# Kernel optimization log

Hardware: AMD Instinct MI355X
Metric: run time of the kernel (lower is better)

Reference implementation:

```python
import jax, jax.numpy as jnp
import numpy as np

B, T, N, F, D, E = 8, 256, 118, 3, 128, 372
G = B * T  # number of graphs after flattening batch*time


def _gcn(x, src, dst, W, b):
    # x: [G, N, Fin] -> PyG GCNConv: X' = D^-1/2 (A+I) D^-1/2 (X W) + b
    h = x @ W  # [G, N, Fout]
    deg = jnp.ones((N,), h.dtype).at[dst].add(1.0)  # in-degree + self loop
    inv = deg ** -0.5
    norm = inv[src] * inv[dst]  # [E]
    agg = h * (1.0 / deg)[None, :, None]  # self-loop term: inv[i]*inv[i] = 1/deg
    agg = agg.at[:, dst].add(h[:, src] * norm[None, :, None])
    return agg + b


def _lstm_layer(x, Wih, Whh, bih, bhh):
    # x: [B, T, I]; PyTorch gate order i, f, g, o
    Bb, H = x.shape[0], Whh.shape[1]
    h0 = jnp.zeros((Bb, H), x.dtype)
    c0 = jnp.zeros((Bb, H), x.dtype)

    def step(carry, xt):
        h, c = carry
        gates = xt @ Wih.T + h @ Whh.T + bih + bhh
        i, f, g, o = jnp.split(gates, 4, axis=-1)
        c = jax.nn.sigmoid(f) * c + jax.nn.sigmoid(i) * jnp.tanh(g)
        h = jax.nn.sigmoid(o) * jnp.tanh(c)
        return (h, c), h

    _, ys = jax.lax.scan(step, (h0, c0), jnp.swapaxes(x, 0, 1))
    return jnp.swapaxes(ys, 0, 1)


def setup_inputs() -> dict:
    key = jax.random.key(0)
    ks = jax.random.split(key, 24)
    s = 0.05

    def rn(i, shape):
        return jax.random.normal(ks[i], shape, jnp.float32) * s

    return {
        "snapshot_sequence": jax.random.normal(ks[0], (B, T, N, F), jnp.float32),
        "edge_index": jax.random.randint(ks[1], (2, E), 0, N, dtype=jnp.int64),
        "scale": jnp.ones((F,), jnp.float32),
        "shift": jnp.zeros((F,), jnp.float32),
        "W1": rn(2, (F, D)), "b1": jnp.zeros((D,), jnp.float32),
        "W2": rn(3, (D, D)), "b2": jnp.zeros((D,), jnp.float32),
        "W3": rn(4, (D, D)), "b3": jnp.zeros((D,), jnp.float32),
        "Wih0": rn(5, (4 * D, D)), "Whh0": rn(6, (4 * D, D)),
        "bih0": jnp.zeros((4 * D,), jnp.float32), "bhh0": jnp.zeros((4 * D,), jnp.float32),
        "Wih1": rn(7, (4 * D, D)), "Whh1": rn(8, (4 * D, D)),
        "bih1": jnp.zeros((4 * D,), jnp.float32), "bhh1": jnp.zeros((4 * D,), jnp.float32),
        "hW1": rn(9, (D, 128)), "hb1": jnp.zeros((128,), jnp.float32),
        "hW2": rn(10, (128, 64)), "hb2": jnp.zeros((64,), jnp.float32),
        "hW3": rn(11, (64, 2)), "hb3": jnp.zeros((2,), jnp.float32),
    }


def reference(snapshot_sequence, edge_index, scale, shift,
              W1, b1, W2, b2, W3, b3,
              Wih0, Whh0, bih0, bhh0, Wih1, Whh1, bih1, bhh1,
              hW1, hb1, hW2, hb2, hW3, hb3):
    src, dst = edge_index[0], edge_index[1]
    x = snapshot_sequence * scale + shift              # FeatureNormalizer
    x = x.reshape(G, N, F)                             # flatten batch*time graphs
    x = jax.nn.silu(_gcn(x, src, dst, W1, b1))         # GCNConv 1 (dropout = eval identity)
    x = jax.nn.silu(_gcn(x, src, dst, W2, b2))         # GCNConv 2
    x = jax.nn.silu(_gcn(x, src, dst, W3, b3))         # GCNConv 3
    emb = x.mean(axis=1)                               # global_mean_pool -> [G, D]
    emb = emb.reshape(B, T, D)
    h = _lstm_layer(emb, Wih0, Whh0, bih0, bhh0)       # 2-layer LSTM (eval: no dropout)
    h = _lstm_layer(h, Wih1, Whh1, bih1, bhh1)
    final = h[:, -1, :]                                # [B, D]
    y = jax.nn.silu(final @ hW1 + hb1)
    y = jax.nn.silu(y @ hW2 + hb2)
    y = y @ hW3 + hb3
    return jax.nn.softplus(y) + 1e-6                   # [B, 2]
```

## Files before the change

### kernel.cpp

```cpp
#include <hip/hip_runtime.h>
#include <math.h>

#define NN 118
#define EE 372
#define GG 2048
#define DD 128
#define TT 256
#define BB 8
#define FD 512

#define XS 136

typedef short bf16x8 __attribute__((ext_vector_type(8)));
typedef float f32x4  __attribute__((ext_vector_type(4)));
typedef _Float16 f16x2 __attribute__((ext_vector_type(2)));

__device__ __forceinline__ float frcp_(float x) { return __builtin_amdgcn_rcpf(x); }
__device__ __forceinline__ float sig_f(float x) { return frcp_(1.0f + __expf(-x)); }
__device__ __forceinline__ float tanh_f(float x) { return 1.0f - 2.0f * frcp_(__expf(2.0f * x) + 1.0f); }
__device__ __forceinline__ float silu_f(float x) { return x * frcp_(1.0f + __expf(-x)); }
__device__ __forceinline__ float siluf_(float x) { return x / (1.0f + expf(-x)); }

__device__ __forceinline__ float fdot2_(unsigned int a, unsigned int b, float c) {
#if defined(__has_builtin) && __has_builtin(__builtin_amdgcn_fdot2)
    return __builtin_amdgcn_fdot2(__builtin_bit_cast(f16x2, a),
                                  __builtin_bit_cast(f16x2, b), c, false);
#else
    f16x2 x = __builtin_bit_cast(f16x2, a), y = __builtin_bit_cast(f16x2, b);
    return c + (float)x[0] * (float)y[0] + (float)x[1] * (float)y[1];
#endif
}

__device__ __forceinline__ void bar_lds() {
    asm volatile("s_waitcnt lgkmcnt(0)\n\ts_barrier" ::: "memory");
}

__device__ __forceinline__ unsigned short f2bf(float x) {
    unsigned int u = __float_as_uint(x);
    unsigned int r = (u + 0x7fffu + ((u >> 16) & 1u)) >> 16;
    return (unsigned short)r;
}
__device__ __forceinline__ float bf2f(unsigned short b) {
    return __uint_as_float(((unsigned int)b) << 16);
}

__global__ void prep_kernel(const int* __restrict__ ei,
                            const float* __restrict__ bih0, const float* __restrict__ bhh0,
                            const float* __restrict__ bih1, const float* __restrict__ bhh1,
                            float* __restrict__ bias0, float* __restrict__ bias1,
                            unsigned short* __restrict__ AbG) {
    __shared__ int sflag;
    __shared__ int ssrc[EE], sdst[EE];
    __shared__ int scount[NN];
    __shared__ float sinv[NN];
    __shared__ float Adense[NN * NN];
    int tid = threadIdx.x;
    if (tid == 0) sflag = 0;
    __syncthreads();
    for (int i = tid; i < 2 * EE; i += blockDim.x)
        if ((i & 1) && ei[i] != 0) atomicOr(&sflag, 1);
    __syncthreads();
    bool m64 = (sflag == 0);
    for (int e = tid; e < EE; e += blockDim.x) {
        int s, d;
        if (m64) { s = ei[2 * e]; d = ei[2 * EE + 2 * e]; }
        else     { s = ei[e];     d = ei[EE + e]; }
        s = min(max(s, 0), NN - 1); d = min(max(d, 0), NN - 1);
        ssrc[e] = s; sdst[e] = d;
    }
    for (int n = tid; n < NN; n += blockDim.x) scount[n] = 0;
    for (int i = tid; i < NN * NN; i += blockDim.x) Adense[i] = 0.0f;
    __syncthreads();
    for (int e = tid; e < EE; e += blockDim.x) atomicAdd(&scount[sdst[e]], 1);
    __syncthreads();
    for (int n = tid; n < NN; n += blockDim.x) {
        float deg = 1.0f + (float)scount[n];
        sinv[n] = rsqrtf(deg);
        Adense[n * NN + n] = 1.0f / deg;
    }
    __syncthreads();
    for (int e = tid; e < EE; e += blockDim.x)
        atomicAdd(&Adense[sdst[e] * NN + ssrc[e]], sinv[ssrc[e]] * sinv[sdst[e]]);
    __syncthreads();
    for (int i = tid; i < 128 * 128; i += blockDim.x) {
        int r = i >> 7, c = i & 127;
        AbG[i] = (r < NN && c < NN) ? f2bf(Adense[r * NN + c]) : (unsigned short)0;
    }
    for (int j = tid; j < FD; j += blockDim.x) {
        bias0[j] = bih0[j] + bhh0[j];
        bias1[j] = bih1[j] + bhh1[j];
    }
}

__global__ void convw_kernel(const float* __restrict__ W, unsigned short* __restrict__ out) {
    int i = blockIdx.x * 512 + threadIdx.x;
    int n = i >> 7, k = i & 127;
    out[i] = f2bf(W[k * DD + n]);
}

__global__ void convh_kernel(const float* __restrict__ W, unsigned int* __restrict__ out) {
    int i = blockIdx.x * 512 + threadIdx.x;
    int d = i & 127;
    int rest = i >> 7;
    int quarter = rest & 3;
    int qg = rest >> 2;
    int q = qg & 15, g = qg >> 4;
    const float* row = W + (size_t)(g * 128 + d) * 128 + quarter * 32;
    float a = row[2 * q], b = row[2 * q + 1];
    unsigned short lo = __builtin_bit_cast(unsigned short, (_Float16)a);
    unsigned short hi = __builtin_bit_cast(unsigned short, (_Float16)b);
    out[i] = (unsigned int)lo | ((unsigned int)hi << 16);
}

__global__ void transpose_kernel(const float* __restrict__ in, float* __restrict__ out) {
    int idx = blockIdx.x * blockDim.x + threadIdx.x;
    int j = idx >> 7, k = idx & 127;
    out[k * FD + j] = in[idx];
}

__device__ __forceinline__ void load_m(const unsigned short* __restrict__ src,
                                       unsigned short* __restrict__ dst, int tid) {
    const uint4* s4 = (const uint4*)src;
    for (int c = tid; c < 2048; c += 512) {
        int r = c >> 4, k8 = (c & 15) * 8;
        uint4 v = s4[c];
        *(uint4*)(dst + r * XS + k8) = v;
    }
}

__device__ __forceinline__ void mm_xw(const unsigned short* __restrict__ xb,
                                      const unsigned short* __restrict__ wt,
                                      unsigned short* __restrict__ hS, int tid) {
    int lane = tid & 63, w = tid >> 6;
    int lm = lane & 15, lq = lane >> 4;
    int wm = (w & 1) * 64, wn = (w >> 1) * 32;
    f32x4 acc[4][2];
#pragma unroll
    for (int mt = 0; mt < 4; ++mt)
#pragma unroll
        for (int nt = 0; nt < 2; ++nt) acc[mt][nt] = (f32x4){0.f, 0.f, 0.f, 0.f};
#pragma unroll
    for (int kb = 0; kb < 4; ++kb) {
        int ko = kb * 32 + lq * 8;
        bf16x8 b0 = *(const bf16x8*)(wt + (wn + lm) * XS + ko);
        bf16x8 b1 = *(const bf16x8*)(wt + (wn + 16 + lm) * XS + ko);
#pragma unroll
        for (int mt = 0; mt < 4; ++mt) {
            bf16x8 af = *(const bf16x8*)(xb + (wm + mt * 16 + lm) * XS + ko);
            acc[mt][0] = __builtin_amdgcn_mfma_f32_16x16x32_bf16(af, b0, acc[mt][0], 0, 0, 0);
            acc[mt][1] = __builtin_amdgcn_mfma_f32_16x16x32_bf16(af, b1, acc[mt][1], 0, 0, 0);
        }
    }
#pragma unroll
    for (int mt = 0; mt < 4; ++mt)
#pragma unroll
        for (int nt = 0; nt < 2; ++nt) {
            f32x4 a = acc[mt][nt];
            ushort4 pk;
            pk.x = f2bf(a[0]); pk.y = f2bf(a[1]); pk.z = f2bf(a[2]); pk.w = f2bf(a[3]);
            *(ushort4*)(hS + (wn + nt * 16 + lm) * XS + wm + mt * 16 + lq * 4) = pk;
        }
}

__device__ __forceinline__ void mm_agg(const unsigned short* __restrict__ Ab,
                                       const unsigned short* __restrict__ hS,
                                       unsigned short* __restrict__ xb,
                                       float bn0, float bn1, int tid) {
    int lane = tid & 63, w = tid >> 6;
    int lm = lane & 15, lq = lane >> 4;
    int wm = (w & 1) * 64, wn = (w >> 1) * 32;
    f32x4 acc[4][2];
#pragma unroll
    for (int mt = 0; mt < 4; ++mt)
#pragma unroll
        for (int nt = 0; nt < 2; ++nt) acc[mt][nt] = (f32x4){0.f, 0.f, 0.f, 0.f};
#pragma unroll
    for (int kb = 0; kb < 4; ++kb) {
        int ko = kb * 32 + lq * 8;
        bf16x8 b0 = *(const bf16x8*)(hS + (wn + lm) * XS + ko);
        bf16x8 b1 = *(const bf16x8*)(hS + (wn + 16 + lm) * XS + ko);
#pragma unroll
        for (int mt = 0; mt < 4; ++mt) {
            bf16x8 af = *(const bf16x8*)(Ab + (wm + mt * 16 + lm) * XS + ko);
            acc[mt][0] = __builtin_amdgcn_mfma_f32_16x16x32_bf16(af, b0, acc[mt][0], 0, 0, 0);
            acc[mt][1] = __builtin_amdgcn_mfma_f32_16x16x32_bf16(af, b1, acc[mt][1], 0, 0, 0);
        }
    }
#pragma unroll
    for (int mt = 0; mt < 4; ++mt)
#pragma unroll
        for (int nt = 0; nt < 2; ++nt) {
            float bn = nt ? bn1 : bn0;
            int col = wn + nt * 16 + lm;
#pragma unroll
            for (int i = 0; i < 4; ++i) {
                float v = silu_f(acc[mt][nt][i] + bn);
                xb[(wm + mt * 16 + lq * 4 + i) * XS + col] = f2bf(v);
            }
        }
}

__global__ __launch_bounds__(512) void gcn_kernel(
    const float* __restrict__ xg, const float* __restrict__ scale, const float* __restrict__ shift,
    const float* __restrict__ W1, const float* __restrict__ b1,
    const float* __restrict__ b2, const float* __restrict__ b3,
    const unsigned short* __restrict__ AbG,
    const unsigned short* __restrict__ Wt2g, const unsigned short* __restrict__ Wt3g,
    float* __restrict__ emb) {
    extern __shared__ char smem[];
    unsigned short* xb = (unsigned short*)smem;
    unsigned short* hS = (unsigned short*)(smem + 34816);
    unsigned short* Ab = (unsigned short*)(smem + 69632);
    unsigned short* wt = (unsigned short*)(smem + 104448);
    float* xinL  = (float*)(smem + 139264);
    float* meanS = (float*)(smem + 140688);
    int tid = threadIdx.x;
    int lane = tid & 63, w = tid >> 6;
    int g = blockIdx.x;

    for (int i = tid; i < 2176; i += 512) ((uint4*)hS)[i] = (uint4){0, 0, 0, 0};
    for (int i = tid; i < 170; i += 512) ((uint4*)(xb + NN * XS))[i] = (uint4){0, 0, 0, 0};
    float s0 = scale[0], s1 = scale[1], s2 = scale[2];
    float t0 = shift[0], t1 = shift[1], t2 = shift[2];
    const float* xrow = xg + (size_t)g * (NN * 3);
    for (int i = tid; i < NN * 3; i += 512) {
        int f = i % 3;
        float sc = (f == 0) ? s0 : ((f == 1) ? s1 : s2);
        float sf = (f == 0) ? t0 : ((f == 1) ? t1 : t2);
        xinL[i] = xrow[i] * sc + sf;
    }
    load_m(AbG, Ab, tid);
    load_m(Wt2g, wt, tid);
    int lm = lane & 15;
    int wn = (w >> 1) * 32;
    int n0 = wn + lm, n1 = wn + 16 + lm;
    float b1a = b1[n0], b1b = b1[n1];
    float b2a = b2[n0], b2b = b2[n1];
    float b3a = b3[n0], b3b = b3[n1];
    int dd = lane * 2;
    float2 w10 = *(const float2*)(W1 + dd);
    float2 w11 = *(const float2*)(W1 + DD + dd);
    float2 w12 = *(const float2*)(W1 + 2 * DD + dd);
    bar_lds();
    for (int k = 0; k < 15; ++k) {
        int n = w + 8 * k;
        if (n >= NN) break;
        float x0 = xinL[n * 3], x1 = xinL[n * 3 + 1], x2 = xinL[n * 3 + 2];
        hS[dd * XS + n]       = f2bf(x0 * w10.x + x1 * w11.x + x2 * w12.x);
        hS[(dd + 1) * XS + n] = f2bf(x0 * w10.y + x1 * w11.y + x2 * w12.y);
    }
    bar_lds();
    mm_agg(Ab, hS, xb, b1a, b1b, tid);
    bar_lds();
    mm_xw(xb, wt, hS, tid);
    bar_lds();
    load_m(Wt3g, wt, tid);
    mm_agg(Ab, hS, xb, b2a, b2b, tid);
    bar_lds();
    mm_xw(xb, wt, hS, tid);
    bar_lds();
    mm_agg(Ab, hS, xb, b3a, b3b, tid);
    bar_lds();
    {
        int d = tid & 127, part = tid >> 7;
        int a0 = part * 30;
        int a1 = (a0 + 30 < NN) ? (a0 + 30) : NN;
        float s = 0.f;
        for (int n = a0; n < a1; ++n) s += bf2f(xb[n * XS + d]);
        meanS[part * 128 + d] = s;
    }
    bar_lds();
    if (tid < 128) {
        float s = meanS[tid] + meanS[128 + tid] + meanS[256 + tid] + meanS[384 + tid];
        emb[(size_t)g * DD + tid] = s * (1.0f / (float)NN);
    }
}

__global__ __launch_bounds__(512) void proj_kernel(const float* __restrict__ src,
                                                   const float* __restrict__ WT,
                                                   const float* __restrict__ bias,
                                                   float* __restrict__ dst) {
    __shared__ __align__(16) float eL[DD];
    int g = blockIdx.x, tid = threadIdx.x;
    if (tid < DD) eL[tid] = src[(size_t)g * DD + tid];
    __syncthreads();
    float acc = bias[tid];
    const float* wt = WT + tid;
#pragma unroll 8
    for (int k = 0; k < DD; ++k) acc += eL[k] * wt[(size_t)k * FD];
    dst[(size_t)g * FD + tid] = acc;
}

__global__ __launch_bounds__(512, 2) void scan_kernel(
    const float* __restrict__ inp,
    const unsigned int* __restrict__ Wc,
    float* __restrict__ hout, int full) {
    __shared__ __align__(16) unsigned short hL[DD];
    __shared__ __align__(16) float sgP[3 * DD * 4];
    int b = blockIdx.x, j = threadIdx.x;
    int d = j & 127, quarter = j >> 7;
    unsigned int wreg[4][16];
#pragma unroll
    for (int g = 0; g < 4; ++g)
#pragma unroll
        for (int q = 0; q < 16; ++q)
            wreg[g][q] = Wc[(((g * 16 + q) << 2) + quarter) * 128 + d];
#pragma unroll
    for (int g = 0; g < 4; ++g)
#pragma unroll
        for (int q = 0; q < 16; ++q)
            asm volatile("" : "+v"(wreg[g][q]));
    if (j < 64) ((unsigned int*)hL)[j] = 0u;
    float creg = 0.f;
    const float* ib = inp + (size_t)b * TT * FD;
    float* hb_ = hout + (size_t)b * (full ? TT * DD : DD);
    float xg0[4], xg1[4];
    if (quarter == 0) {
#pragma unroll
        for (int g = 0; g < 4; ++g) { xg0[g] = ib[g * DD + d]; xg1[g] = ib[FD + g * DD + d]; }
    }
    bar_lds();
    for (int t = 0; t < TT; ++t) {
        float xg2[4];
        if (quarter == 0) {
            bool more = (t + 2 < TT);
#pragma unroll
            for (int g = 0; g < 4; ++g)
                xg2[g] = more ? ib[(t + 2) * FD + g * DD + d] : 0.f;
        }
        const uint4* h4 = (const uint4*)(hL + quarter * 32);
        float a0 = 0.f, a1 = 0.f, a2 = 0.f, a3 = 0.f;
#pragma unroll
        for (int c = 0; c < 4; ++c) {
            uint4 hv = h4[c];
            a0 = fdot2_(wreg[0][4 * c + 0], hv.x, a0);
            a1 = fdot2_(wreg[1][4 * c + 0], hv.x, a1);
            a2 = fdot2_(wreg[2][4 * c + 0], hv.x, a2);
            a3 = fdot2_(wreg[3][4 * c + 0], hv.x, a3);
            a0 = fdot2_(wreg[0][4 * c + 1], hv.y, a0);
            a1 = fdot2_(wreg[1][4 * c + 1], hv.y, a1);
            a2 = fdot2_(wreg[2][4 * c + 1], hv.y, a2);
            a3 = fdot2_(wreg[3][4 * c + 1], hv.y, a3);
            a0 = fdot2_(wreg[0][4 * c + 2], hv.z, a0);
            a1 = fdot2_(wreg[1][4 * c + 2], hv.z, a1);
            a2 = fdot2_(wreg[2][4 * c + 2], hv.z, a2);
            a3 = fdot2_(wreg[3][4 * c + 2], hv.z, a3);
            a0 = fdot2_(wreg[0][4 * c + 3], hv.w, a0);
            a1 = fdot2_(wreg[1][4 * c + 3], hv.w, a1);
            a2 = fdot2_(wreg[2][4 * c + 3], hv.w, a2);
            a3 = fdot2_(wreg[3][4 * c + 3], hv.w, a3);
        }
        if (quarter != 0)
            *(float4*)(sgP + ((quarter - 1) * DD + d) * 4) = make_float4(a0, a1, a2, a3);
        bar_lds();
        if (quarter == 0) {
            float4 p1 = *(const float4*)(sgP + d * 4);
            float4 p2 = *(const float4*)(sgP + (DD + d) * 4);
            float4 p3 = *(const float4*)(sgP + (2 * DD + d) * 4);
            float iv = sig_f(a0 + p1.x + p2.x + p3.x + xg0[0]);
            float fv = sig_f(a1 + p1.y + p2.y + p3.y + xg0[1]);
            float gv = tanh_f(a2 + p1.z + p2.z + p3.z + xg0[2]);
            float ov = sig_f(a3 + p1.w + p2.w + p3.w + xg0[3]);
            float cn = fv * creg + iv * gv;
            creg = cn;
            float hn = ov * tanh_f(cn);
            ((_Float16*)hL)[d] = (_Float16)hn;
            if (full) hb_[t * DD + d] = hn;
            else if (t == TT - 1) hb_[d] = hn;
#pragma unroll
            for (int g = 0; g < 4; ++g) { xg0[g] = xg1[g]; xg1[g] = xg2[g]; }
        }
        bar_lds();
    }
}

__global__ void head_kernel(const float* __restrict__ hfin,
                            const float* __restrict__ hW1, const float* __restrict__ hb1,
                            const float* __restrict__ hW2, const float* __restrict__ hb2,
                            const float* __restrict__ hW3, const float* __restrict__ hb3,
                            float* __restrict__ out) {
    __shared__ float fh[BB * DD];
    __shared__ float y1[BB * DD];
    __shared__ float y2[BB * 64];
    int tid = threadIdx.x;
    for (int i = tid; i < BB * DD; i += 256) fh[i] = hfin[i];
    __syncthreads();
    for (int i = tid; i < BB * DD; i += 256) {
        int bb = i >> 7, jj = i & 127;
        float acc = hb1[jj];
        for (int k = 0; k < DD; ++k) acc += fh[(bb << 7) + k] * hW1[(k << 7) + jj];
        y1[i] = siluf_(acc);
    }
    __syncthreads();
    for (int i = tid; i < BB * 64; i += 256) {
        int bb = i >> 6, jj = i & 63;
        float acc = hb2[jj];
        for (int k = 0; k < DD; ++k) acc += y1[(bb << 7) + k] * hW2[(k << 6) + jj];
        y2[i] = siluf_(acc);
    }
    __syncthreads();
    if (tid < BB * 2) {
        int bb = tid >> 1, m = tid & 1;
        float acc = hb3[m];
        for (int k = 0; k < 64; ++k) acc += y2[(bb << 6) + k] * hW3[k * 2 + m];
        float sp = fmaxf(acc, 0.f) + log1pf(expf(-fabsf(acc)));
        out[tid] = sp + 1e-6f;
    }
}

extern "C" void kernel_launch(void* const* d_in, const int* in_sizes, int n_in,
                              void* d_out, int out_size, void* d_ws, size_t ws_size,
                              hipStream_t stream) {
    const float* snap  = (const float*)d_in[0];
    const int*   edges = (const int*)d_in[1];
    const float* scale = (const float*)d_in[2];
    const float* shift = (const float*)d_in[3];
    const float* W1 = (const float*)d_in[4];
    const float* b1 = (const float*)d_in[5];
    const float* W2 = (const float*)d_in[6];
    const float* b2 = (const float*)d_in[7];
    const float* W3 = (const float*)d_in[8];
    const float* b3 = (const float*)d_in[9];
    const float* Wih0 = (const float*)d_in[10];
    const float* Whh0 = (const float*)d_in[11];
    const float* bih0 = (const float*)d_in[12];
    const float* bhh0 = (const float*)d_in[13];
    const float* Wih1 = (const float*)d_in[14];
    const float* Whh1 = (const float*)d_in[15];
    const float* bih1 = (const float*)d_in[16];
    const float* bhh1 = (const float*)d_in[17];
    const float* hW1 = (const float*)d_in[18];
    const float* hb1 = (const float*)d_in[19];
    const float* hW2 = (const float*)d_in[20];
    const float* hb2 = (const float*)d_in[21];
    const float* hW3 = (const float*)d_in[22];
    const float* hb3 = (const float*)d_in[23];

    float* ws = (float*)d_ws;
    float* bias0 = ws + 0;
    float* bias1 = ws + 512;
    unsigned short* AbG  = (unsigned short*)(ws + 1024);
    unsigned short* Wt2g = (unsigned short*)(ws + 9216);
    unsigned short* Wt3g = (unsigned short*)(ws + 17408);
    float* WT0 = ws + 25600;
    float* WT1 = ws + 91136;
    unsigned int* Wc0 = (unsigned int*)(ws + 156672);
    unsigned int* Wc1 = (unsigned int*)(ws + 189440);
    float* emb   = ws + 222208;
    float* inp   = ws + 484352;
    float* h0seq = ws + 1532928;
    float* hfin  = ws + 1795072;

    const int smem_gcn = 142736;
    hipFuncSetAttribute((const void*)gcn_kernel,
                        hipFuncAttributeMaxDynamicSharedMemorySize, smem_gcn);

    prep_kernel<<<1, 256, 0, stream>>>(edges, bih0, bhh0, bih1, bhh1,
                                       bias0, bias1, AbG);
    convw_kernel<<<32, 512, 0, stream>>>(W2, Wt2g);
    convw_kernel<<<32, 512, 0, stream>>>(W3, Wt3g);
    convh_kernel<<<64, 512, 0, stream>>>(Whh0, Wc0);
    convh_kernel<<<64, 512, 0, stream>>>(Whh1, Wc1);
    transpose_kernel<<<128, 512, 0, stream>>>(Wih0, WT0);
    transpose_kernel<<<128, 512, 0, stream>>>(Wih1, WT1);
    gcn_kernel<<<GG, 512, smem_gcn, stream>>>(snap, scale, shift, W1, b1, b2, b3,
                                              AbG, Wt2g, Wt3g, emb);
    proj_kernel<<<GG, 512, 0, stream>>>(emb, WT0, bias0, inp);
    scan_kernel<<<BB, 512, 0, stream>>>(inp, Wc0, h0seq, 1);
    proj_kernel<<<GG, 512, 0, stream>>>(h0seq, WT1, bias1, inp);
    scan_kernel<<<BB, 512, 0, stream>>>(inp, Wc1, hfin, 0);
    head_kernel<<<1, 256, 0, stream>>>(hfin, hW1, hb1, hW2, hb2, hW3, hb3, (float*)d_out);
}
```

Measured before the change: 582.0 us.

## Reduce LSTM gate partials with lane shuffles and double-buffer hidden state

The scan kernel now places the four K-quarters of each hidden unit in adjacent lanes and reduces the gate partial sums with xor shuffles instead of an LDS scratch buffer. This removes one barrier per timestep. The hidden state is double-buffered so the write of h(t+1) cannot race with reads of h(t). The weight packing kernel is reindexed to match the new lane mapping, and only one in four lanes does the gate math, so the nonlinearity phase becomes spread across more waves.

```diff
diff --git a/kernel.cpp b/kernel.cpp
--- a/kernel.cpp
+++ b/kernel.cpp
@@ -100,11 +100,10 @@
 
 __global__ void convh_kernel(const float* __restrict__ W, unsigned int* __restrict__ out) {
     int i = blockIdx.x * 512 + threadIdx.x;
-    int d = i & 127;
-    int rest = i >> 7;
-    int quarter = rest & 3;
-    int qg = rest >> 2;
-    int q = qg & 15, g = qg >> 4;
+    int j = i & 511;
+    int quarter = j & 3, d = j >> 2;
+    int gq = i >> 9;
+    int q = gq & 15, g = gq >> 4;
     const float* row = W + (size_t)(g * 128 + d) * 128 + quarter * 32;
     float a = row[2 * q], b = row[2 * q + 1];
     unsigned short lo = __builtin_bit_cast(unsigned short, (_Float16)a);
@@ -295,22 +294,21 @@
     const float* __restrict__ inp,
     const unsigned int* __restrict__ Wc,
     float* __restrict__ hout, int full) {
-    __shared__ __align__(16) unsigned short hL[DD];
-    __shared__ __align__(16) float sgP[3 * DD * 4];
+    __shared__ __align__(16) unsigned short hL[2][DD];
     int b = blockIdx.x, j = threadIdx.x;
-    int d = j & 127, quarter = j >> 7;
+    int quarter = j & 3, d = j >> 2;
     unsigned int wreg[4][16];
 #pragma unroll
     for (int g = 0; g < 4; ++g)
 #pragma unroll
         for (int q = 0; q < 16; ++q)
-            wreg[g][q] = Wc[(((g * 16 + q) << 2) + quarter) * 128 + d];
+            wreg[g][q] = Wc[(g * 16 + q) * 512 + j];
 #pragma unroll
     for (int g = 0; g < 4; ++g)
 #pragma unroll
         for (int q = 0; q < 16; ++q)
             asm volatile("" : "+v"(wreg[g][q]));
-    if (j < 64) ((unsigned int*)hL)[j] = 0u;
+    if (j < 128) ((unsigned int*)hL)[j] = 0u;
     float creg = 0.f;
     const float* ib = inp + (size_t)b * TT * FD;
     float* hb_ = hout + (size_t)b * (full ? TT * DD : DD);
@@ -328,7 +326,7 @@
             for (int g = 0; g < 4; ++g)
                 xg2[g] = more ? ib[(t + 2) * FD + g * DD + d] : 0.f;
         }
-        const uint4* h4 = (const uint4*)(hL + quarter * 32);
+        const uint4* h4 = (const uint4*)(hL[t & 1] + quarter * 32);
         float a0 = 0.f, a1 = 0.f, a2 = 0.f, a3 = 0.f;
 #pragma unroll
         for (int c = 0; c < 4; ++c) {
@@ -350,21 +348,19 @@
             a2 = fdot2_(wreg[2][4 * c + 3], hv.w, a2);
             a3 = fdot2_(wreg[3][4 * c + 3], hv.w, a3);
         }
-        if (quarter != 0)
-            *(float4*)(sgP + ((quarter - 1) * DD + d) * 4) = make_float4(a0, a1, a2, a3);
-        bar_lds();
+        a0 += __shfl_xor(a0, 1); a0 += __shfl_xor(a0, 2);
+        a1 += __shfl_xor(a1, 1); a1 += __shfl_xor(a1, 2);
+        a2 += __shfl_xor(a2, 1); a2 += __shfl_xor(a2, 2);
+        a3 += __shfl_xor(a3, 1); a3 += __shfl_xor(a3, 2);
         if (quarter == 0) {
-            float4 p1 = *(const float4*)(sgP + d * 4);
-            float4 p2 = *(const float4*)(sgP + (DD + d) * 4);
-            float4 p3 = *(const float4*)(sgP + (2 * DD + d) * 4);
-            float iv = sig_f(a0 + p1.x + p2.x + p3.x + xg0[0]);
-            float fv = sig_f(a1 + p1.y + p2.y + p3.y + xg0[1]);
-            float gv = tanh_f(a2 + p1.z + p2.z + p3.z + xg0[2]);
-            float ov = sig_f(a3 + p1.w + p2.w + p3.w + xg0[3]);
+            float iv = sig_f(a0 + xg0[0]);
+            float fv = sig_f(a1 + xg0[1]);
+            float gv = tanh_f(a2 + xg0[2]);
+            float ov = sig_f(a3 + xg0[3]);
             float cn = fv * creg + iv * gv;
             creg = cn;
             float hn = ov * tanh_f(cn);
-            ((_Float16*)hL)[d] = (_Float16)hn;
+            ((_Float16*)hL[(t + 1) & 1])[d] = (_Float16)hn;
             if (full) hb_[t * DD + d] = hn;
             else if (t == TT - 1) hb_[d] = hn;
 #pragma unroll
```

Result: slower. 653.1 us (+12.2%).
